# Performance work log

Hardware: AMD Instinct MI355X
Metric: run time of the kernel (lower is better)

## Reference

```python
import jax, jax.numpy as jnp
import numpy as np

B, IN, F, HID, D, RH, OUT, C, R = 4096, 1024, 512, 128, 128, 64, 1, 10, 16


def setup_inputs() -> dict:
    key = jax.random.key(0)
    ks = jax.random.split(key, 24)
    def p(k, shape, s=0.05):
        return jax.random.normal(k, shape, jnp.float32) * s
    return {
        'x': jax.random.normal(ks[0], (B, IN), jnp.float32),
        'pref': jax.random.uniform(ks[1], (R, 2), jnp.float32),
        'base_w': p(ks[2], (F, IN)), 'base_b': p(ks[3], (F,)),
        'wm1_w': p(ks[4], (16, 2)), 'wm1_b': p(ks[5], (16,)),
        'wm2_w': p(ks[6], (C, 16)), 'wm2_b': p(ks[7], (C,)),
        'ray0_w': p(ks[8], (C, RH, 2)), 'ray0_b': p(ks[9], (C, RH)),
        'ray2_w': p(ks[10], (C, D, RH)), 'ray2_b': p(ks[11], (C, D)),
        'fc1_w': p(ks[12], (C, HID * F, D)), 'fc1_b': p(ks[13], (C, HID * F)),
        'b1_w': p(ks[14], (C, HID, D)), 'b1_b': p(ks[15], (C, HID)),
        'fc2_w': p(ks[16], (C, OUT * HID, D)), 'fc2_b': p(ks[17], (C, OUT * HID)),
        'b2_w': p(ks[18], (C, OUT, D)), 'b2_b': p(ks[19], (C, OUT)),
    }


def reference(x, pref, base_w, base_b, wm1_w, wm1_b, wm2_w, wm2_b,
              ray0_w, ray0_b, ray2_w, ray2_b, fc1_w, fc1_b,
              b1_w, b1_b, fc2_w, fc2_b, b2_w, b2_b):
    # base feature extractor: (B, F)
    feature = x @ base_w.T + base_b
    # client mixing weights per ray: (R, C), normalized over clients
    h = jax.nn.relu(pref @ wm1_w.T + wm1_b)
    w = jax.nn.sigmoid(h @ wm2_w.T + wm2_b)
    w = w / jnp.sum(w, axis=1, keepdims=True)
    # merged ray-MLP (nonlinear -> merge the tiny weights explicitly per ray)
    m0w = jnp.einsum('rc,cod->rod', w, ray0_w)          # (R, RH, 2)
    r1 = jax.nn.relu(jnp.einsum('rd,rod->ro', pref, m0w) + w @ ray0_b)
    m2w = jnp.einsum('rc,coh->roh', w, ray2_w)          # (R, D, RH)
    ray2v = jnp.einsum('rh,roh->ro', r1, m2w) + w @ ray2_b  # (R, D)

    def hyper(Wc, bc):
        # sum_c w[r,c] * (ray2v[r] @ Wc[c].T + bc[c])  == F.linear with merged params
        per_client = jnp.einsum('rd,cod->rco', ray2v, Wc)   # (R, C, O)
        return jnp.einsum('rc,rco->ro', w, per_client) + w @ bc

    W1 = hyper(fc1_w, fc1_b).reshape(R, HID, F)   # generated layer-1 weight
    b1 = hyper(b1_w, b1_b)                        # (R, HID)
    W2 = hyper(fc2_w, fc2_b).reshape(R, OUT, HID) # generated layer-2 weight
    b2 = hyper(b2_w, b2_b)                        # (R, OUT)

    v1 = jnp.einsum('bf,rhf->rbh', feature, W1) + b1[:, None, :]  # (R, B, HID)
    out = jnp.einsum('rbh,roh->rbo', v1, W2) + b2[:, None, :]     # (R, B, OUT)
    return jax.nn.sigmoid(out), out
```

## Files before the change

### kernel.cpp

```cpp
#include <hip/hip_runtime.h>
#include <cstddef>
#include <cstdint>


#define WS_WT    0
#define WS_RV    160
#define WS_W2T   2208
#define WS_WEFF  4256
#define WS_WFIN  12448
#define WS_BFIN  28832
#define WS_R1    28848
#define WS_ZERO_BEG WS_WEFF
#define WS_ZERO_CNT (WS_BFIN + 16 - WS_WEFF)

__device__ __forceinline__ void load_coef(const float* __restrict__ WT,
                                          const float* __restrict__ W2T,
                                          int c, int h, float* cw) {
  const float4* wc4 = (const float4*)(WT + c * 16);
  const float4* w24 = (const float4*)(W2T + h * 16);
  float4 a0 = wc4[0], a1 = wc4[1], a2 = wc4[2], a3 = wc4[3];
  float4 c0 = w24[0], c1 = w24[1], c2 = w24[2], c3 = w24[3];
  cw[0]  = a0.x * c0.x; cw[1]  = a0.y * c0.y; cw[2]  = a0.z * c0.z; cw[3]  = a0.w * c0.w;
  cw[4]  = a1.x * c1.x; cw[5]  = a1.y * c1.y; cw[6]  = a1.z * c1.z; cw[7]  = a1.w * c1.w;
  cw[8]  = a2.x * c2.x; cw[9]  = a2.y * c2.y; cw[10] = a2.z * c2.z; cw[11] = a2.w * c2.w;
  cw[12] = a3.x * c3.x; cw[13] = a3.y * c3.y; cw[14] = a3.z * c3.z; cw[15] = a3.w * c3.w;
}

__global__ __launch_bounds__(256) void k_front(
    const float* __restrict__ pref, const float* __restrict__ wm1_w,
    const float* __restrict__ wm1_b, const float* __restrict__ wm2_w,
    const float* __restrict__ wm2_b, const float* __restrict__ ray0_w,
    const float* __restrict__ ray0_b, const float* __restrict__ ray2_b,
    const float* __restrict__ fc2_b, float* __restrict__ ws) {
  __shared__ float sh1[16][16];
  __shared__ float sw[16][10];
  __shared__ float sinv[16];
  const int t = threadIdx.x;
  {
    int r = t >> 4, j = t & 15;
    float v = pref[r * 2 + 0] * wm1_w[j * 2 + 0] + pref[r * 2 + 1] * wm1_w[j * 2 + 1] + wm1_b[j];
    sh1[r][j] = fmaxf(v, 0.f);
  }
  __syncthreads();
  if (t < 160) {
    int r = t / 10, c = t % 10;
    float z = wm2_b[c];
    for (int j = 0; j < 16; ++j) z += sh1[r][j] * wm2_w[c * 16 + j];
    sw[r][c] = 1.f / (1.f + expf(-z));
  }
  __syncthreads();
  if (t < 16) {
    float s = 0.f;
    for (int c = 0; c < 10; ++c) s += sw[t][c];
    sinv[t] = 1.f / s;
  }
  __syncthreads();
  if (t < 160) {
    int r = t / 10, c = t % 10;
    float v = sw[r][c] * sinv[r];
    sw[r][c] = v;
    ws[WS_WT + c * 16 + r] = v;
  }
  __syncthreads();
  for (int it = t; it < 1024; it += 256) {
    int r = it >> 6, o = it & 63;
    float m0 = 0.f, m1 = 0.f, rb = 0.f;
    for (int c = 0; c < 10; ++c) {
      float wv = sw[r][c];
      m0 += wv * ray0_w[(c * 64 + o) * 2 + 0];
      m1 += wv * ray0_w[(c * 64 + o) * 2 + 1];
      rb += wv * ray0_b[c * 64 + o];
    }
    float v = pref[r * 2 + 0] * m0 + pref[r * 2 + 1] * m1 + rb;
    ws[WS_R1 + it] = fmaxf(v, 0.f);
  }
  for (int it = t; it < 2048; it += 256) {
    int r = it >> 7, d = it & 127;
    float a = 0.f;
    for (int c = 0; c < 10; ++c) a += sw[r][c] * ray2_b[c * 128 + d];
    ws[WS_RV + it] = a;
  }
  for (int it = t; it < 2048; it += 256) {
    int h = it >> 4, r = it & 15;
    float a = 0.f;
    for (int c = 0; c < 10; ++c) a += sw[r][c] * fc2_b[c * 128 + h];
    ws[WS_W2T + it] = a;
  }
}

__global__ __launch_bounds__(256) void k_rv(const float* __restrict__ ray2_w,
                                            float* __restrict__ ws) {
  __shared__ float r1s[16 * 65];
  const int t = threadIdx.x;
  for (int k = t; k < 1024; k += 256) r1s[(k >> 6) * 65 + (k & 63)] = ws[WS_R1 + k];
  __syncthreads();
  const int tid = blockIdx.x * 256 + t;
  const int r = tid & 15;
  const int pair = tid >> 4;
  const float4* row4 = (const float4*)(ray2_w + (size_t)pair * 64);
  const float* r1r = r1s + r * 65;
  float dot = 0.f;
#pragma unroll
  for (int k = 0; k < 16; ++k) {
    float4 a = row4[k];
    dot += a.x * r1r[k * 4 + 0] + a.y * r1r[k * 4 + 1] + a.z * r1r[k * 4 + 2] + a.w * r1r[k * 4 + 3];
  }
  int c = pair >> 7, d = pair & 127;
  atomicAdd(&ws[WS_RV + r * 128 + d], ws[WS_WT + c * 16 + r] * dot);
}

__global__ __launch_bounds__(256) void k_w2(const float* __restrict__ fc2_w,
                                            float* __restrict__ ws) {
  const int t = threadIdx.x;
  const int lane = t & 63;
  const int wave = __builtin_amdgcn_readfirstlane(blockIdx.x * 4 + (t >> 6));
  float2 rv2[16];
#pragma unroll
  for (int r = 0; r < 16; ++r) rv2[r] = *(const float2*)&ws[WS_RV + r * 128 + lane * 2];
  for (int q = 0; q < 4; ++q) {
    int rid = wave * 4 + q;
    int c = rid >> 7, h = rid & 127;
    float2 a = *(const float2*)&fc2_w[(size_t)rid * 128 + lane * 2];
    float u[16];
#pragma unroll
    for (int r = 0; r < 16; ++r) {
      float tt = a.x * rv2[r].x + a.y * rv2[r].y;
      u[r] = tt * ws[WS_WT + c * 16 + r];
    }
#pragma unroll
    for (int m = 1; m <= 4; m <<= 1) {
#pragma unroll
      for (int r = 0; r < 16; ++r) u[r] += __shfl_xor(u[r], m, 64);
    }
    if ((lane & 7) == 0) {
#pragma unroll
      for (int r = 0; r < 16; ++r) atomicAdd(&ws[WS_W2T + h * 16 + r], u[r]);
    }
  }
}

__global__ __launch_bounds__(256, 3) void k_main(
    const float* __restrict__ fc1_w, const float* __restrict__ fc1_b,
    const float* __restrict__ b1_w, const float* __restrict__ b1_b,
    const float* __restrict__ b2_w, const float* __restrict__ b2_b,
    float* __restrict__ ws) {
  const int blk = blockIdx.x;
  const int t = threadIdx.x;
  const float* WT = ws + WS_WT;
  const float* W2T = ws + WS_W2T;
  const float* RV = ws + WS_RV;

  if (blk < 1024) {
    const int lane = t & 63;
    const int wave = __builtin_amdgcn_readfirstlane(blk * 4 + (t >> 6));
    const int fp = wave & 255;
    const int ch0 = (wave >> 8) * 80;
    const int l32 = lane & 31;
    float4 rvq[16];
#pragma unroll
    for (int r = 0; r < 16; ++r) rvq[r] = *(const float4*)&RV[r * 128 + l32 * 4];
    float acc[16];
#pragma unroll
    for (int r = 0; r < 16; ++r) acc[r] = 0.f;

    const float4* p = (const float4*)fc1_w + (size_t)ch0 * 16384 + fp * 64 + lane;

    auto sstep = [&](const float4& av, int ch) {
      int c = ch >> 7, h = ch & 127;
      float cw[16];
      load_coef(WT, W2T, c, h, cw);
#pragma unroll
      for (int r = 0; r < 16; ++r) {
        float tt = av.x * rvq[r].x + av.y * rvq[r].y + av.z * rvq[r].z + av.w * rvq[r].w;
        acc[r] = fmaf(cw[r], tt, acc[r]);
      }
    };

    float4 a = *p; p += 16384;
    for (int it = 0; it < 79; ++it) {
      float4 an = *p; p += 16384;
      sstep(a, ch0 + it);
      a = an;
    }
    sstep(a, ch0 + 79);

#pragma unroll
    for (int m = 1; m <= 16; m <<= 1) {
#pragma unroll
      for (int r = 0; r < 16; ++r) acc[r] += __shfl_xor(acc[r], m, 64);
    }
    if (l32 == 0) {
      const int f = fp * 2 + (lane >> 5);
#pragma unroll
      for (int r = 0; r < 16; ++r) atomicAdd(&ws[WS_WEFF + r * 512 + f], acc[r]);
    }
  } else if (blk < 1040) {
    const int bb = blk - 1024;
    const int f = (bb & 1) * 256 + t;
    const int ch0 = __builtin_amdgcn_readfirstlane((bb >> 1) * 160);
    float acc[16];
#pragma unroll
    for (int r = 0; r < 16; ++r) acc[r] = 0.f;
    for (int it = 0; it < 160; ++it) {
      const int ch = ch0 + it;
      const int c = ch >> 7, h = ch & 127;
      float xb = fc1_b[(size_t)c * 65536 + h * 512 + f];
      float cw[16];
      load_coef(WT, W2T, c, h, cw);
#pragma unroll
      for (int r = 0; r < 16; ++r) acc[r] = fmaf(cw[r], xb, acc[r]);
    }
#pragma unroll
    for (int r = 0; r < 16; ++r) atomicAdd(&ws[WS_WEFF + r * 512 + f], acc[r]);
  } else {
    const int lane = t & 63;
    const int wave = __builtin_amdgcn_readfirstlane((blk - 1040) * 4 + (t >> 6));
    float2 rv2[16];
#pragma unroll
    for (int r = 0; r < 16; ++r) rv2[r] = *(const float2*)&RV[r * 128 + lane * 2];
    float acc[16];
#pragma unroll
    for (int r = 0; r < 16; ++r) acc[r] = 0.f;
    const int ch0 = wave * 160;
    for (int it = 0; it < 160; ++it) {
      const int ch = ch0 + it;
      const int c = ch >> 7, h = ch & 127;
      float2 a = *(const float2*)&b1_w[(size_t)ch * 128 + lane * 2];
      float cw[16];
      load_coef(WT, W2T, c, h, cw);
#pragma unroll
      for (int r = 0; r < 16; ++r)
        acc[r] = fmaf(cw[r], a.x * rv2[r].x + a.y * rv2[r].y, acc[r]);
    }
#pragma unroll
    for (int m = 1; m <= 32; m <<= 1) {
#pragma unroll
      for (int r = 0; r < 16; ++r) acc[r] += __shfl_xor(acc[r], m, 64);
    }
    if (lane == 0) {
#pragma unroll
      for (int r = 0; r < 16; ++r) atomicAdd(&ws[WS_BFIN + r], acc[r]);
    }
    if (wave == 7) {
      float a2[16];
#pragma unroll
      for (int r = 0; r < 16; ++r) a2[r] = 0.f;
      for (int i = lane; i < 1280; i += 64) {
        int c = i >> 7, h = i & 127;
        float v = b1_b[c * 128 + h];
#pragma unroll
        for (int r = 0; r < 16; ++r)
          a2[r] = fmaf(WT[c * 16 + r] * W2T[h * 16 + r], v, a2[r]);
      }
      for (int i = lane; i < 1280; i += 64) {
        int c = i >> 7, d = i & 127;
        float v = b2_w[c * 128 + d];
#pragma unroll
        for (int r = 0; r < 16; ++r)
          a2[r] = fmaf(WT[c * 16 + r] * RV[r * 128 + d], v, a2[r]);
      }
      if (lane < 10) {
        float v = b2_b[lane];
#pragma unroll
        for (int r = 0; r < 16; ++r) a2[r] = fmaf(WT[lane * 16 + r], v, a2[r]);
      }
#pragma unroll
      for (int m = 1; m <= 32; m <<= 1) {
#pragma unroll
        for (int r = 0; r < 16; ++r) a2[r] += __shfl_xor(a2[r], m, 64);
      }
      if (lane == 0) {
#pragma unroll
        for (int r = 0; r < 16; ++r) atomicAdd(&ws[WS_BFIN + r], a2[r]);
      }
    }
  }
}

__global__ __launch_bounds__(256) void k_wfin(const float* __restrict__ base_w,
                                              const float* __restrict__ base_b,
                                              float* __restrict__ ws) {
  const int t = threadIdx.x;
  const int blk = blockIdx.x;
  const int i = (blk & 3) * 256 + t;
  const int f0 = __builtin_amdgcn_readfirstlane((blk >> 2) * 32);
  const float* WEFF = ws + WS_WEFF;
  float acc[16];
#pragma unroll
  for (int r = 0; r < 16; ++r) acc[r] = 0.f;
#pragma unroll 4
  for (int f = f0; f < f0 + 32; ++f) {
    float bw = base_w[(size_t)f * 1024 + i];
#pragma unroll
    for (int r = 0; r < 16; ++r) acc[r] = fmaf(WEFF[r * 512 + f], bw, acc[r]);
  }
#pragma unroll
  for (int r = 0; r < 16; ++r) atomicAdd(&ws[WS_WFIN + r * 1024 + i], acc[r]);

  if (blk == 0 && t < 64) {
    float a2[16];
#pragma unroll
    for (int r = 0; r < 16; ++r) a2[r] = 0.f;
    for (int f = t; f < 512; f += 64) {
      float v = base_b[f];
#pragma unroll
      for (int r = 0; r < 16; ++r) a2[r] = fmaf(WEFF[r * 512 + f], v, a2[r]);
    }
#pragma unroll
    for (int m = 1; m <= 32; m <<= 1) {
#pragma unroll
      for (int r = 0; r < 16; ++r) a2[r] += __shfl_xor(a2[r], m, 64);
    }
    if (t == 0) {
#pragma unroll
      for (int r = 0; r < 16; ++r) atomicAdd(&ws[WS_BFIN + r], a2[r]);
    }
  }
}

__global__ __launch_bounds__(256) void k_out(const float* __restrict__ x,
                                             const float* __restrict__ ws,
                                             float* __restrict__ out) {
  __shared__ float4 wfs[4096];
  const int t = threadIdx.x;
  const float4* wf4 = (const float4*)(ws + WS_WFIN);
#pragma unroll
  for (int k = 0; k < 16; ++k) wfs[t + 256 * k] = wf4[t + 256 * k];
  __syncthreads();

  const int b0 = blockIdx.x * 16;
  const int bp = t >> 5;
  const int isub = t & 31;
  const int bA = b0 + bp * 2;
  const float* xa = x + (size_t)bA * 1024;
  const float* xb = xa + 1024;
  float acc0[16], acc1[16];
#pragma unroll
  for (int r = 0; r < 16; ++r) { acc0[r] = 0.f; acc1[r] = 0.f; }

  for (int chunk = 0; chunk < 4; ++chunk) {
#pragma unroll
    for (int j = 0; j < 2; ++j) {
      const int off = chunk * 256 + j * 128 + isub * 4;
      float4 xv0 = *(const float4*)&xa[off];
      float4 xv1 = *(const float4*)&xb[off];
      const float4* wrow = wfs + chunk * 64 + j * 32 + isub;
#pragma unroll
      for (int r = 0; r < 16; ++r) {
        float4 w = wrow[r * 256];
        acc0[r] += xv0.x * w.x + xv0.y * w.y + xv0.z * w.z + xv0.w * w.w;
        acc1[r] += xv1.x * w.x + xv1.y * w.y + xv1.z * w.z + xv1.w * w.w;
      }
    }
  }
#pragma unroll
  for (int m = 1; m <= 16; m <<= 1) {
#pragma unroll
    for (int r = 0; r < 16; ++r) {
      acc0[r] += __shfl_xor(acc0[r], m, 64);
      acc1[r] += __shfl_xor(acc1[r], m, 64);
    }
  }
  if (isub == 0) {
#pragma unroll
    for (int r = 0; r < 16; ++r) {
      float bf = ws[WS_BFIN + r];
      float v0 = acc0[r] + bf;
      float v1 = acc1[r] + bf;
      out[r * 4096 + bA] = 1.f / (1.f + expf(-v0));
      out[r * 4096 + bA + 1] = 1.f / (1.f + expf(-v1));
      out[65536 + r * 4096 + bA] = v0;
      out[65536 + r * 4096 + bA + 1] = v1;
    }
  }
}

extern "C" void kernel_launch(void* const* d_in, const int* in_sizes, int n_in,
                              void* d_out, int out_size, void* d_ws, size_t ws_size,
                              hipStream_t stream) {
  (void)in_sizes; (void)n_in; (void)out_size; (void)ws_size;
  const float* x      = (const float*)d_in[0];
  const float* pref   = (const float*)d_in[1];
  const float* base_w = (const float*)d_in[2];
  const float* base_b = (const float*)d_in[3];
  const float* wm1_w  = (const float*)d_in[4];
  const float* wm1_b  = (const float*)d_in[5];
  const float* wm2_w  = (const float*)d_in[6];
  const float* wm2_b  = (const float*)d_in[7];
  const float* ray0_w = (const float*)d_in[8];
  const float* ray0_b = (const float*)d_in[9];
  const float* ray2_w = (const float*)d_in[10];
  const float* ray2_b = (const float*)d_in[11];
  const float* fc1_w  = (const float*)d_in[12];
  const float* fc1_b  = (const float*)d_in[13];
  const float* b1_w   = (const float*)d_in[14];
  const float* b1_b   = (const float*)d_in[15];
  const float* fc2_w  = (const float*)d_in[16];
  const float* fc2_b  = (const float*)d_in[17];
  const float* b2_w   = (const float*)d_in[18];
  const float* b2_b   = (const float*)d_in[19];
  float* ws  = (float*)d_ws;
  float* out = (float*)d_out;

  hipMemsetAsync(ws + WS_ZERO_BEG, 0, (size_t)WS_ZERO_CNT * sizeof(float), stream);
  k_front<<<1, 256, 0, stream>>>(pref, wm1_w, wm1_b, wm2_w, wm2_b,
                                 ray0_w, ray0_b, ray2_b, fc2_b, ws);
  k_rv<<<80, 256, 0, stream>>>(ray2_w, ws);
  k_w2<<<80, 256, 0, stream>>>(fc2_w, ws);
  k_main<<<1042, 256, 0, stream>>>(fc1_w, fc1_b, b1_w, b1_b, b2_w, b2_b, ws);
  k_wfin<<<64, 256, 0, stream>>>(base_w, base_b, ws);
  k_out<<<256, 256, 0, stream>>>(x, ws, out);
}
```

Before: 651.1 us.

## Fuse front kernels, split fc1 reduction across more blocks with shared coefficients

Merges the front MLP and ray2 projection into one 80-block kernel that recomputes the mixing weights per block, which removes one launch and the workspace round trip for r1. The main fc1 streaming kernel now uses twice as many blocks with 40 channels each. Per-channel coefficient products are precomputed into shared memory, and fc1 loads are prefetched three deep. The bias paths get their own block groups with block-level reductions before the atomics, and k_wfin doubles its grid. This adds redundant front computation in every block and more atomics on WEFF.

```diff
diff --git a/kernel.cpp b/kernel.cpp
--- a/kernel.cpp
+++ b/kernel.cpp
@@ -9,32 +9,16 @@
 #define WS_WEFF  4256
 #define WS_WFIN  12448
 #define WS_BFIN  28832
-#define WS_R1    28848
-#define WS_ZERO_BEG WS_WEFF
-#define WS_ZERO_CNT (WS_BFIN + 16 - WS_WEFF)
-
-__device__ __forceinline__ void load_coef(const float* __restrict__ WT,
-                                          const float* __restrict__ W2T,
-                                          int c, int h, float* cw) {
-  const float4* wc4 = (const float4*)(WT + c * 16);
-  const float4* w24 = (const float4*)(W2T + h * 16);
-  float4 a0 = wc4[0], a1 = wc4[1], a2 = wc4[2], a3 = wc4[3];
-  float4 c0 = w24[0], c1 = w24[1], c2 = w24[2], c3 = w24[3];
-  cw[0]  = a0.x * c0.x; cw[1]  = a0.y * c0.y; cw[2]  = a0.z * c0.z; cw[3]  = a0.w * c0.w;
-  cw[4]  = a1.x * c1.x; cw[5]  = a1.y * c1.y; cw[6]  = a1.z * c1.z; cw[7]  = a1.w * c1.w;
-  cw[8]  = a2.x * c2.x; cw[9]  = a2.y * c2.y; cw[10] = a2.z * c2.z; cw[11] = a2.w * c2.w;
-  cw[12] = a3.x * c3.x; cw[13] = a3.y * c3.y; cw[14] = a3.z * c3.z; cw[15] = a3.w * c3.w;
-}
-
-__global__ __launch_bounds__(256) void k_front(
-    const float* __restrict__ pref, const float* __restrict__ wm1_w,
-    const float* __restrict__ wm1_b, const float* __restrict__ wm2_w,
-    const float* __restrict__ wm2_b, const float* __restrict__ ray0_w,
-    const float* __restrict__ ray0_b, const float* __restrict__ ray2_b,
-    const float* __restrict__ fc2_b, float* __restrict__ ws) {
-  __shared__ float sh1[16][16];
-  __shared__ float sw[16][10];
-  __shared__ float sinv[16];
+#define WS_ZERO_BEG WS_RV
+#define WS_ZERO_CNT (WS_BFIN + 16 - WS_RV)
+
+__device__ __forceinline__ void front_mlp(const float* __restrict__ pref,
+                                          const float* __restrict__ wm1_w,
+                                          const float* __restrict__ wm1_b,
+                                          const float* __restrict__ wm2_w,
+                                          const float* __restrict__ wm2_b,
+                                          float (*sh1)[16], float (*sw)[10],
+                                          float* sinv) {
   const int t = threadIdx.x;
   {
     int r = t >> 4, j = t & 15;
@@ -57,11 +41,24 @@
   __syncthreads();
   if (t < 160) {
     int r = t / 10, c = t % 10;
-    float v = sw[r][c] * sinv[r];
-    sw[r][c] = v;
-    ws[WS_WT + c * 16 + r] = v;
-  }
-  __syncthreads();
+    sw[r][c] = sw[r][c] * sinv[r];
+  }
+  __syncthreads();
+}
+
+__global__ __launch_bounds__(256) void k_stage1(
+    const float* __restrict__ pref, const float* __restrict__ wm1_w,
+    const float* __restrict__ wm1_b, const float* __restrict__ wm2_w,
+    const float* __restrict__ wm2_b, const float* __restrict__ ray0_w,
+    const float* __restrict__ ray0_b, const float* __restrict__ ray2_w,
+    const float* __restrict__ ray2_b, const float* __restrict__ fc2_b,
+    float* __restrict__ ws) {
+  __shared__ float sh1[16][16];
+  __shared__ float sw[16][10];
+  __shared__ float sinv[16];
+  __shared__ float r1s[16][65];
+  const int t = threadIdx.x;
+  front_mlp(pref, wm1_w, wm1_b, wm2_w, wm2_b, sh1, sw, sinv);
   for (int it = t; it < 1024; it += 256) {
     int r = it >> 6, o = it & 63;
     float m0 = 0.f, m1 = 0.f, rb = 0.f;
@@ -72,69 +69,61 @@
       rb += wv * ray0_b[c * 64 + o];
     }
     float v = pref[r * 2 + 0] * m0 + pref[r * 2 + 1] * m1 + rb;
-    ws[WS_R1 + it] = fmaxf(v, 0.f);
-  }
-  for (int it = t; it < 2048; it += 256) {
-    int r = it >> 7, d = it & 127;
-    float a = 0.f;
-    for (int c = 0; c < 10; ++c) a += sw[r][c] * ray2_b[c * 128 + d];
-    ws[WS_RV + it] = a;
-  }
-  for (int it = t; it < 2048; it += 256) {
-    int h = it >> 4, r = it & 15;
-    float a = 0.f;
-    for (int c = 0; c < 10; ++c) a += sw[r][c] * fc2_b[c * 128 + h];
-    ws[WS_W2T + it] = a;
-  }
-}
-
-__global__ __launch_bounds__(256) void k_rv(const float* __restrict__ ray2_w,
-                                            float* __restrict__ ws) {
-  __shared__ float r1s[16 * 65];
-  const int t = threadIdx.x;
-  for (int k = t; k < 1024; k += 256) r1s[(k >> 6) * 65 + (k & 63)] = ws[WS_R1 + k];
-  __syncthreads();
-  const int tid = blockIdx.x * 256 + t;
-  const int r = tid & 15;
-  const int pair = tid >> 4;
-  const float4* row4 = (const float4*)(ray2_w + (size_t)pair * 64);
-  const float* r1r = r1s + r * 65;
+    r1s[r][o] = fmaxf(v, 0.f);
+  }
+  __syncthreads();
+  const int pair = blockIdx.x * 16 + (t >> 4);
+  const int r = t & 15;
+  const float* row = ray2_w + (size_t)pair * 64;
+  const float* r1r = r1s[r];
   float dot = 0.f;
 #pragma unroll
-  for (int k = 0; k < 16; ++k) {
-    float4 a = row4[k];
-    dot += a.x * r1r[k * 4 + 0] + a.y * r1r[k * 4 + 1] + a.z * r1r[k * 4 + 2] + a.w * r1r[k * 4 + 3];
-  }
+  for (int k = 0; k < 64; ++k) dot += row[k] * r1r[k];
   int c = pair >> 7, d = pair & 127;
-  atomicAdd(&ws[WS_RV + r * 128 + d], ws[WS_WT + c * 16 + r] * dot);
-}
-
-__global__ __launch_bounds__(256) void k_w2(const float* __restrict__ fc2_w,
-                                            float* __restrict__ ws) {
+  atomicAdd(&ws[WS_RV + r * 128 + d], sw[r][c] * dot);
+
+  if (blockIdx.x == 0) {
+    if (t < 160) ws[WS_WT + t] = sw[t & 15][t >> 4];
+    for (int i = t; i < 2048; i += 256) {
+      int rr = i >> 7, dd = i & 127;
+      float s = 0.f;
+      for (int cc = 0; cc < 10; ++cc) s += sw[rr][cc] * ray2_b[cc * 128 + dd];
+      atomicAdd(&ws[WS_RV + i], s);
+    }
+  } else if (blockIdx.x == 1) {
+    for (int i = t; i < 2048; i += 256) {
+      int h = i >> 4, rr = i & 15;
+      float s = 0.f;
+      for (int cc = 0; cc < 10; ++cc) s += sw[rr][cc] * fc2_b[cc * 128 + h];
+      atomicAdd(&ws[WS_W2T + i], s);
+    }
+  }
+}
+
+__global__ __launch_bounds__(256) void k_stage2(const float* __restrict__ fc2_w,
+                                                float* __restrict__ ws) {
   const int t = threadIdx.x;
   const int lane = t & 63;
-  const int wave = __builtin_amdgcn_readfirstlane(blockIdx.x * 4 + (t >> 6));
+  const int wv = blockIdx.x * 4 + (t >> 6);
   float2 rv2[16];
 #pragma unroll
   for (int r = 0; r < 16; ++r) rv2[r] = *(const float2*)&ws[WS_RV + r * 128 + lane * 2];
   for (int q = 0; q < 4; ++q) {
-    int rid = wave * 4 + q;
+    int rid = wv * 4 + q;
     int c = rid >> 7, h = rid & 127;
     float2 a = *(const float2*)&fc2_w[(size_t)rid * 128 + lane * 2];
     float u[16];
 #pragma unroll
-    for (int r = 0; r < 16; ++r) {
-      float tt = a.x * rv2[r].x + a.y * rv2[r].y;
-      u[r] = tt * ws[WS_WT + c * 16 + r];
-    }
-#pragma unroll
-    for (int m = 1; m <= 4; m <<= 1) {
+    for (int r = 0; r < 16; ++r) u[r] = a.x * rv2[r].x + a.y * rv2[r].y;
+#pragma unroll
+    for (int m = 1; m <= 32; m <<= 1) {
 #pragma unroll
       for (int r = 0; r < 16; ++r) u[r] += __shfl_xor(u[r], m, 64);
     }
-    if ((lane & 7) == 0) {
-#pragma unroll
-      for (int r = 0; r < 16; ++r) atomicAdd(&ws[WS_W2T + h * 16 + r], u[r]);
+    if (lane == 0) {
+#pragma unroll
+      for (int r = 0; r < 16; ++r)
+        atomicAdd(&ws[WS_W2T + h * 16 + r], u[r] * ws[WS_WT + c * 16 + r]);
     }
   }
 }
@@ -144,46 +133,46 @@
     const float* __restrict__ b1_w, const float* __restrict__ b1_b,
     const float* __restrict__ b2_w, const float* __restrict__ b2_b,
     float* __restrict__ ws) {
+  __shared__ float scoef[2560];
+  __shared__ float bfred[4][16];
   const int blk = blockIdx.x;
   const int t = threadIdx.x;
-  const float* WT = ws + WS_WT;
-  const float* W2T = ws + WS_W2T;
-  const float* RV = ws + WS_RV;
-
-  if (blk < 1024) {
-    const int lane = t & 63;
-    const int wave = __builtin_amdgcn_readfirstlane(blk * 4 + (t >> 6));
-    const int fp = wave & 255;
-    const int ch0 = (wave >> 8) * 80;
-    const int l32 = lane & 31;
-    float4 rvq[16];
-#pragma unroll
-    for (int r = 0; r < 16; ++r) rvq[r] = *(const float4*)&RV[r * 128 + l32 * 4];
+
+  if (blk < 2048) {
+    const int wid = t >> 6, lane = t & 63, l32 = lane & 31;
+    const int ch0 = (blk >> 6) * 40;
+    const int fp = (blk & 63) * 4 + wid;
+    for (int i = t; i < 640; i += 256) {
+      int chl = i >> 4, r = i & 15;
+      int ch = ch0 + chl, c = ch >> 7, h = ch & 127;
+      scoef[i] = ws[WS_WT + c * 16 + r] * ws[WS_W2T + h * 16 + r];
+    }
+    __syncthreads();
+    float4 rv[16];
+#pragma unroll
+    for (int r = 0; r < 16; ++r) rv[r] = *(const float4*)&ws[WS_RV + r * 128 + l32 * 4];
     float acc[16];
 #pragma unroll
     for (int r = 0; r < 16; ++r) acc[r] = 0.f;
 
     const float4* p = (const float4*)fc1_w + (size_t)ch0 * 16384 + fp * 64 + lane;
-
-    auto sstep = [&](const float4& av, int ch) {
-      int c = ch >> 7, h = ch & 127;
-      float cw[16];
-      load_coef(WT, W2T, c, h, cw);
+    float4 a0 = p[0];
+    float4 a1 = p[16384];
+    float4 a2 = p[2 * 16384];
+    p += (size_t)3 * 16384;
+    for (int chl = 0; chl < 40; ++chl) {
+      float4 cur = a0; a0 = a1; a1 = a2;
+      if (chl < 37) { a2 = *p; p += 16384; }
+      const float4* cf = (const float4*)(scoef + chl * 16);
+      float4 c0 = cf[0], c1 = cf[1], c2 = cf[2], c3 = cf[3];
+      float cw[16] = {c0.x, c0.y, c0.z, c0.w, c1.x, c1.y, c1.z, c1.w,
+                      c2.x, c2.y, c2.z, c2.w, c3.x, c3.y, c3.z, c3.w};
 #pragma unroll
       for (int r = 0; r < 16; ++r) {
-        float tt = av.x * rvq[r].x + av.y * rvq[r].y + av.z * rvq[r].z + av.w * rvq[r].w;
+        float tt = cur.x * rv[r].x + cur.y * rv[r].y + cur.z * rv[r].z + cur.w * rv[r].w;
         acc[r] = fmaf(cw[r], tt, acc[r]);
       }
-    };
-
-    float4 a = *p; p += 16384;
-    for (int it = 0; it < 79; ++it) {
-      float4 an = *p; p += 16384;
-      sstep(a, ch0 + it);
-      a = an;
-    }
-    sstep(a, ch0 + 79);
-
+    }
 #pragma unroll
     for (int m = 1; m <= 16; m <<= 1) {
 #pragma unroll
@@ -194,43 +183,100 @@
 #pragma unroll
       for (int r = 0; r < 16; ++r) atomicAdd(&ws[WS_WEFF + r * 512 + f], acc[r]);
     }
-  } else if (blk < 1040) {
-    const int bb = blk - 1024;
+  } else if (blk < 2064) {
+    const int bb = blk - 2048;
     const int f = (bb & 1) * 256 + t;
-    const int ch0 = __builtin_amdgcn_readfirstlane((bb >> 1) * 160);
+    const int ch0 = (bb >> 1) * 160;
+    for (int i = t; i < 2560; i += 256) {
+      int chl = i >> 4, r = i & 15;
+      int ch = ch0 + chl, c = ch >> 7, h = ch & 127;
+      scoef[i] = ws[WS_WT + c * 16 + r] * ws[WS_W2T + h * 16 + r];
+    }
+    __syncthreads();
     float acc[16];
 #pragma unroll
     for (int r = 0; r < 16; ++r) acc[r] = 0.f;
+    const float* q = fc1_b + (size_t)ch0 * 512 + f;
+    float x0 = q[0], x1 = q[512];
+    q += 1024;
     for (int it = 0; it < 160; ++it) {
-      const int ch = ch0 + it;
-      const int c = ch >> 7, h = ch & 127;
-      float xb = fc1_b[(size_t)c * 65536 + h * 512 + f];
-      float cw[16];
-      load_coef(WT, W2T, c, h, cw);
-#pragma unroll
-      for (int r = 0; r < 16; ++r) acc[r] = fmaf(cw[r], xb, acc[r]);
+      float xv = x0; x0 = x1;
+      if (it < 158) { x1 = q[0]; q += 512; }
+      const float4* cf = (const float4*)(scoef + it * 16);
+      float4 c0 = cf[0], c1 = cf[1], c2 = cf[2], c3 = cf[3];
+      float cw[16] = {c0.x, c0.y, c0.z, c0.w, c1.x, c1.y, c1.z, c1.w,
+                      c2.x, c2.y, c2.z, c2.w, c3.x, c3.y, c3.z, c3.w};
+#pragma unroll
+      for (int r = 0; r < 16; ++r) acc[r] = fmaf(cw[r], xv, acc[r]);
     }
 #pragma unroll
     for (int r = 0; r < 16; ++r) atomicAdd(&ws[WS_WEFF + r * 512 + f], acc[r]);
+  } else if (blk < 2072) {
+    const int hb = blk - 2064;
+    const int wid = t >> 6, lane = t & 63;
+    const int ch0b = hb * 160;
+    for (int i = t; i < 2560; i += 256) {
+      int chl = i >> 4, r = i & 15;
+      int ch = ch0b + chl, c = ch >> 7, h = ch & 127;
+      scoef[i] = ws[WS_WT + c * 16 + r] * ws[WS_W2T + h * 16 + r];
+    }
+    __syncthreads();
+    float2 rv2[16];
+#pragma unroll
+    for (int r = 0; r < 16; ++r) rv2[r] = *(const float2*)&ws[WS_RV + r * 128 + lane * 2];
+    float acc[16];
+#pragma unroll
+    for (int r = 0; r < 16; ++r) acc[r] = 0.f;
+    const int chl0 = wid * 40;
+    const float2* q = (const float2*)b1_w + (size_t)(ch0b + chl0) * 64 + lane;
+    float2 a0 = q[0], a1 = q[64];
+    q += 128;
+    for (int it = 0; it < 40; ++it) {
+      float2 cur = a0; a0 = a1;
+      if (it < 38) { a1 = q[0]; q += 64; }
+      const float4* cf = (const float4*)(scoef + (chl0 + it) * 16);
+      float4 c0 = cf[0], c1 = cf[1], c2 = cf[2], c3 = cf[3];
+      float cw[16] = {c0.x, c0.y, c0.z, c0.w, c1.x, c1.y, c1.z, c1.w,
+                      c2.x, c2.y, c2.z, c2.w, c3.x, c3.y, c3.z, c3.w};
+#pragma unroll
+      for (int r = 0; r < 16; ++r)
+        acc[r] = fmaf(cw[r], cur.x * rv2[r].x + cur.y * rv2[r].y, acc[r]);
+    }
+#pragma unroll
+    for (int m = 1; m <= 32; m <<= 1) {
+#pragma unroll
+      for (int r = 0; r < 16; ++r) acc[r] += __shfl_xor(acc[r], m, 64);
+    }
+    if (lane == 0) {
+#pragma unroll
+      for (int r = 0; r < 16; ++r) bfred[wid][r] = acc[r];
+    }
+    __syncthreads();
+    if (t < 16)
+      atomicAdd(&ws[WS_BFIN + t], bfred[0][t] + bfred[1][t] + bfred[2][t] + bfred[3][t]);
   } else {
-    const int lane = t & 63;
-    const int wave = __builtin_amdgcn_readfirstlane((blk - 1040) * 4 + (t >> 6));
-    float2 rv2[16];
-#pragma unroll
-    for (int r = 0; r < 16; ++r) rv2[r] = *(const float2*)&RV[r * 128 + lane * 2];
+    const int wid = t >> 6, lane = t & 63;
     float acc[16];
 #pragma unroll
     for (int r = 0; r < 16; ++r) acc[r] = 0.f;
-    const int ch0 = wave * 160;
-    for (int it = 0; it < 160; ++it) {
-      const int ch = ch0 + it;
-      const int c = ch >> 7, h = ch & 127;
-      float2 a = *(const float2*)&b1_w[(size_t)ch * 128 + lane * 2];
-      float cw[16];
-      load_coef(WT, W2T, c, h, cw);
+    for (int i = t; i < 1280; i += 256) {
+      int c = i >> 7, h = i & 127;
+      float v = b1_b[c * 128 + h];
 #pragma unroll
       for (int r = 0; r < 16; ++r)
-        acc[r] = fmaf(cw[r], a.x * rv2[r].x + a.y * rv2[r].y, acc[r]);
+        acc[r] = fmaf(ws[WS_WT + c * 16 + r] * ws[WS_W2T + h * 16 + r], v, acc[r]);
+    }
+    for (int i = t; i < 1280; i += 256) {
+      int c = i >> 7, d = i & 127;
+      float v = b2_w[c * 128 + d];
+#pragma unroll
+      for (int r = 0; r < 16; ++r)
+        acc[r] = fmaf(ws[WS_WT + c * 16 + r] * ws[WS_RV + r * 128 + d], v, acc[r]);
+    }
+    if (t < 10) {
+      float v = b2_b[t];
+#pragma unroll
+      for (int r = 0; r < 16; ++r) acc[r] = fmaf(ws[WS_WT + t * 16 + r], v, acc[r]);
     }
 #pragma unroll
     for (int m = 1; m <= 32; m <<= 1) {
@@ -239,41 +285,11 @@
     }
     if (lane == 0) {
 #pragma unroll
-      for (int r = 0; r < 16; ++r) atomicAdd(&ws[WS_BFIN + r], acc[r]);
-    }
-    if (wave == 7) {
-      float a2[16];
-#pragma unroll
-      for (int r = 0; r < 16; ++r) a2[r] = 0.f;
-      for (int i = lane; i < 1280; i += 64) {
-        int c = i >> 7, h = i & 127;
-        float v = b1_b[c * 128 + h];
-#pragma unroll
-        for (int r = 0; r < 16; ++r)
-          a2[r] = fmaf(WT[c * 16 + r] * W2T[h * 16 + r], v, a2[r]);
-      }
-      for (int i = lane; i < 1280; i += 64) {
-        int c = i >> 7, d = i & 127;
-        float v = b2_w[c * 128 + d];
-#pragma unroll
-        for (int r = 0; r < 16; ++r)
-          a2[r] = fmaf(WT[c * 16 + r] * RV[r * 128 + d], v, a2[r]);
-      }
-      if (lane < 10) {
-        float v = b2_b[lane];
-#pragma unroll
-        for (int r = 0; r < 16; ++r) a2[r] = fmaf(WT[lane * 16 + r], v, a2[r]);
-      }
-#pragma unroll
-      for (int m = 1; m <= 32; m <<= 1) {
-#pragma unroll
-        for (int r = 0; r < 16; ++r) a2[r] += __shfl_xor(a2[r], m, 64);
-      }
-      if (lane == 0) {
-#pragma unroll
-        for (int r = 0; r < 16; ++r) atomicAdd(&ws[WS_BFIN + r], a2[r]);
-      }
-    }
+      for (int r = 0; r < 16; ++r) bfred[wid][r] = acc[r];
+    }
+    __syncthreads();
+    if (t < 16)
+      atomicAdd(&ws[WS_BFIN + t], bfred[0][t] + bfred[1][t] + bfred[2][t] + bfred[3][t]);
   }
 }
 
@@ -283,13 +299,13 @@
   const int t = threadIdx.x;
   const int blk = blockIdx.x;
   const int i = (blk & 3) * 256 + t;
-  const int f0 = __builtin_amdgcn_readfirstlane((blk >> 2) * 32);
+  const int f0 = (blk >> 2) * 16;
   const float* WEFF = ws + WS_WEFF;
   float acc[16];
 #pragma unroll
   for (int r = 0; r < 16; ++r) acc[r] = 0.f;
 #pragma unroll 4
-  for (int f = f0; f < f0 + 32; ++f) {
+  for (int f = f0; f < f0 + 16; ++f) {
     float bw = base_w[(size_t)f * 1024 + i];
 #pragma unroll
     for (int r = 0; r < 16; ++r) acc[r] = fmaf(WEFF[r * 512 + f], bw, acc[r]);
@@ -403,11 +419,10 @@
   float* out = (float*)d_out;
 
   hipMemsetAsync(ws + WS_ZERO_BEG, 0, (size_t)WS_ZERO_CNT * sizeof(float), stream);
-  k_front<<<1, 256, 0, stream>>>(pref, wm1_w, wm1_b, wm2_w, wm2_b,
-                                 ray0_w, ray0_b, ray2_b, fc2_b, ws);
-  k_rv<<<80, 256, 0, stream>>>(ray2_w, ws);
-  k_w2<<<80, 256, 0, stream>>>(fc2_w, ws);
-  k_main<<<1042, 256, 0, stream>>>(fc1_w, fc1_b, b1_w, b1_b, b2_w, b2_b, ws);
-  k_wfin<<<64, 256, 0, stream>>>(base_w, base_b, ws);
+  k_stage1<<<80, 256, 0, stream>>>(pref, wm1_w, wm1_b, wm2_w, wm2_b,
+                                   ray0_w, ray0_b, ray2_w, ray2_b, fc2_b, ws);
+  k_stage2<<<80, 256, 0, stream>>>(fc2_w, ws);
+  k_main<<<2073, 256, 0, stream>>>(fc1_w, fc1_b, b1_w, b1_b, b2_w, b2_b, ws);
+  k_wfin<<<128, 256, 0, stream>>>(base_w, base_b, ws);
   k_out<<<256, 256, 0, stream>>>(x, ws, out);
 }
```

Measured after the change: 566.4 us. 1.15x faster.
